# Kernel optimization log

Hardware: AMD Instinct MI355X
Metric: run time of the kernel (lower is better)

## Reference

```python
import jax, jax.numpy as jnp
import numpy as np

ALPHA = 0.15
KSIZE = 5
EPS = 1e-6


def _minmax_norm(x):
    # x: [B,1,H,W]; per-sample min-max normalize, 0.5 if nearly constant
    mn = x.min(axis=(1, 2, 3), keepdims=True)
    mx = x.max(axis=(1, 2, 3), keepdims=True)
    denom = mx - mn
    safe = jnp.where(denom > EPS, denom, 1.0)
    return jnp.where(denom > EPS, (x - mn) / safe, 0.5)


def _saliency_map(images, out_hw):
    # grayscale via luma weights
    w = jnp.array([0.299, 0.587, 0.114], dtype=images.dtype).reshape(1, 3, 1, 1)
    gray = (images * w).sum(axis=1, keepdims=True)  # [B,1,H,W]
    kernel = jnp.ones((1, 1, KSIZE, KSIZE), dtype=gray.dtype) / (KSIZE * KSIZE)
    dn = ('NCHW', 'OIHW', 'NCHW')
    local_mean = jax.lax.conv_general_dilated(gray, kernel, (1, 1), 'SAME', dimension_numbers=dn)
    local_mean_sq = jax.lax.conv_general_dilated(gray ** 2, kernel, (1, 1), 'SAME', dimension_numbers=dn)
    local_var = jnp.maximum(local_mean_sq - local_mean ** 2, 0.0)
    sal = _minmax_norm(local_var)
    if sal.shape[-2:] != out_hw:
        sal = jax.image.resize(sal, (sal.shape[0], 1, out_hw[0], out_hw[1]), method='bilinear')
    return jax.lax.stop_gradient(sal)  # computed under no_grad / detached in torch


def setup_inputs() -> dict:
    key = jax.random.key(0)
    k1, k2 = jax.random.split(key)
    features = jax.random.normal(k1, (64, 512, 28, 28), dtype=jnp.float32)
    images = jax.random.uniform(k2, (64, 3, 224, 224), dtype=jnp.float32)
    return {"features": features, "images": images}


def reference(features, images):
    sal = _saliency_map(images, features.shape[-2:])  # [B,1,Hf,Wf]
    attn = jnp.sqrt((features ** 2).mean(axis=1, keepdims=True))  # [B,1,Hf,Wf]
    attn = _minmax_norm(attn)
    loss = jnp.mean((attn - sal) ** 2)
    return ALPHA * loss
```

## Files before the change

kernel.cpp:

```cpp
#include <hip/hip_runtime.h>
#include <math.h>

#define BATCH 64
#define HIMG 224
#define WIMG 224
#define IMGPLANE (HIMG*WIMG)
#define CF 512
#define HF 28
#define WF 28
#define POS (HF*WF)
#define ALPHA_C 0.15f
#define EPS_C 1e-6f

#define STRIPS 14
#define SROWS 16
#define GROWS 20
#define GCOLS 228
#define GSTR 229
#define VSTR 261
#define SHN 4580

#define NATTN 512
#define NVARH (STRIPS*BATCH)

#define OFF_HRES 0
#define HRES_CNT (BATCH*HIMG*WF)
#define OFF_BMM (OFF_HRES + HRES_CNT)
#define OFF_AP  (OFF_BMM + BATCH*STRIPS*2)
#define OFF_ACC (OFF_AP + 8*BATCH*POS)
#define OFF_CNT (OFF_ACC + 1)

__global__ __launch_bounds__(256, 2) void fat_k(const float* __restrict__ img,
                                                const float* __restrict__ f,
                                                float* __restrict__ ws) {
    __shared__ float sh[SHN];
    __shared__ float wred[8];
    int bid = blockIdx.x;
    int tid = threadIdx.x;
    int g11 = bid / 11, r11 = bid - 11 * g11;

    if (r11 < 4) {
        int ab = g11 * 4 + r11;
        if (ab == 0 && tid == 0) {
            ws[OFF_ACC] = 0.0f;
            ((unsigned*)ws)[OFF_CNT] = 0u;
        }
        if (tid >= 196) return;
        int b = ab >> 3, z = ab & 7;
        const float* fp = f + (size_t)(b * CF + z * 64) * POS + 4 * tid;
        float ax = 0.0f, ay = 0.0f, az = 0.0f, aw = 0.0f;
        #pragma unroll
        for (int cc = 0; cc < 64; cc += 16) {
            float4 u[16];
            #pragma unroll
            for (int j = 0; j < 16; j++)
                u[j] = *(const float4*)(fp + (size_t)(cc + j) * POS);
            #pragma unroll
            for (int j = 0; j < 16; j++) {
                ax += u[j].x * u[j].x; ay += u[j].y * u[j].y;
                az += u[j].z * u[j].z; aw += u[j].w * u[j].w;
            }
        }
        float4 o = make_float4(ax, ay, az, aw);
        *(float4*)(ws + OFF_AP + (size_t)(z * BATCH + b) * POS + 4 * tid) = o;
        return;
    }

    int vb = g11 * 7 + (r11 - 4);
    int b = vb / STRIPS, sy = vb - b * STRIPS;
    int y0 = sy * SROWS;
    const float* imb = img + (size_t)b * 3 * IMGPLANE;

    for (int i = tid; i < GROWS * 56; i += 256) {
        int gr = i / 56, q = i - gr * 56;
        int gy = y0 - 2 + gr;
        float gx0 = 0.0f, gx1 = 0.0f, gx2 = 0.0f, gx3 = 0.0f;
        if ((unsigned)gy < HIMG) {
            const float* row = imb + gy * WIMG + 4 * q;
            float4 a = *(const float4*)(row);
            float4 bb = *(const float4*)(row + IMGPLANE);
            float4 c = *(const float4*)(row + 2 * IMGPLANE);
            gx0 = 0.299f * a.x + 0.587f * bb.x + 0.114f * c.x;
            gx1 = 0.299f * a.y + 0.587f * bb.y + 0.114f * c.y;
            gx2 = 0.299f * a.z + 0.587f * bb.z + 0.114f * c.z;
            gx3 = 0.299f * a.w + 0.587f * bb.w + 0.114f * c.w;
        }
        int base = gr * GSTR + 2 + 4 * q;
        sh[base] = gx0; sh[base + 1] = gx1; sh[base + 2] = gx2; sh[base + 3] = gx3;
    }
    if (tid < GROWS * 4) {
        int gr = tid >> 2, p = tid & 3;
        int gc = (p < 2) ? p : (224 + p);
        sh[gr * GSTR + gc] = 0.0f;
    }
    __syncthreads();

    int r = tid >> 4, s = tid & 15;
    int x0 = 14 * s;
    const float* gr0 = sh + r * GSTR;
    float c1[5], c2[5], vreg[14];
    #pragma unroll
    for (int m = 0; m < 5; m++) {
        float a = 0.0f, a2 = 0.0f;
        #pragma unroll
        for (int k = 0; k < 5; k++) {
            float u = gr0[k * GSTR + x0 + m];
            a += u; a2 += u * u;
        }
        c1[m] = a; c2[m] = a2;
    }
    float vmn = INFINITY, vmx = 0.0f;
    #pragma unroll
    for (int xi = 0; xi < 14; xi++) {
        int p = xi % 5;
        float s1 = c1[p], s2 = c2[p];
        #pragma unroll
        for (int m = 1; m < 5; m++) {
            s1 += c1[(p + m) % 5];
            s2 += c2[(p + m) % 5];
        }
        float m1 = s1 * 0.04f, m2 = s2 * 0.04f;
        float vv = fmaxf(m2 - m1 * m1, 0.0f);
        vreg[xi] = vv;
        vmn = fminf(vmn, vv); vmx = fmaxf(vmx, vv);
        if (xi < 13) {
            float a = 0.0f, a2 = 0.0f;
            #pragma unroll
            for (int k = 0; k < 5; k++) {
                float u = gr0[k * GSTR + x0 + xi + 5];
                a += u; a2 += u * u;
            }
            c1[p] = a; c2[p] = a2;
        }
    }
    #pragma unroll
    for (int o = 32; o > 0; o >>= 1) {
        vmn = fminf(vmn, __shfl_xor(vmn, o));
        vmx = fmaxf(vmx, __shfl_xor(vmx, o));
    }
    __syncthreads();
    int w = tid >> 6;
    if ((tid & 63) == 0) { wred[w] = vmn; wred[4 + w] = vmx; }
    if (tid < SROWS * 8) {
        int rr = tid >> 3, p = tid & 7;
        int jh = p + ((p < 4) ? 0 : 224);
        sh[rr * VSTR + jh + (jh >> 3)] = 0.0f;
    }
    #pragma unroll
    for (int xi = 0; xi < 14; xi++) {
        int jh = x0 + xi + 4;
        sh[r * VSTR + jh + (jh >> 3)] = vreg[xi];
    }
    __syncthreads();
    if (tid == 0) {
        float mn = fminf(fminf(wred[0], wred[1]), fminf(wred[2], wred[3]));
        float mx = fmaxf(fmaxf(wred[4], wred[5]), fmaxf(wred[6], wred[7]));
        int blk = b * STRIPS + sy;
        ws[OFF_BMM + 2 * blk]     = mn;
        ws[OFF_BMM + 2 * blk + 1] = mx;
    }

    float* hb = ws + OFF_HRES + ((size_t)b * HIMG + y0) * WF;
    for (int idx = tid; idx < SROWS * WF; idx += 256) {
        int rr = idx / WF, i = idx - rr * WF;
        float acc = 0.0f, wsum = 0.0f;
        int j0 = 8 * i - 4;
        #pragma unroll
        for (int t = 0; t < 16; t++) {
            int j = j0 + t;
            float w_ = 8.0f - fabsf((float)t - 7.5f);
            int jh = j + 4;
            acc += w_ * sh[rr * VSTR + jh + (jh >> 3)];
            if ((unsigned)j < WIMG) wsum += w_;
        }
        hb[idx] = acc / wsum;
    }
}

__global__ __launch_bounds__(256) void fused_k(float* __restrict__ ws,
                                               float* __restrict__ out) {
    __shared__ float hres[HIMG][WF + 1];
    __shared__ float wred[4];
    __shared__ float s_mn, s_mx;
    int b = blockIdx.x;
    int tid = threadIdx.x;

    if (tid < 64) {
        float mn = INFINITY, mx = 0.0f;
        if (tid < STRIPS) {
            mn = ws[OFF_BMM + 2 * (b * STRIPS + tid)];
            mx = ws[OFF_BMM + 2 * (b * STRIPS + tid) + 1];
        }
        #pragma unroll
        for (int o = 8; o > 0; o >>= 1) {
            mn = fminf(mn, __shfl_down(mn, o));
            mx = fmaxf(mx, __shfl_down(mx, o));
        }
        if (tid == 0) { s_mn = mn; s_mx = mx; }
    }

    const float* hg = ws + OFF_HRES + (size_t)b * HIMG * WF;
    for (int i = tid; i < HIMG * WF; i += 256) {
        int y = i / WF, x = i - y * WF;
        hres[y][x] = hg[i];
    }
    __syncthreads();

    float vmn = s_mn, vmx = s_mx;
    float vden = vmx - vmn;
    bool vok = vden > EPS_C;

    const float* ap = ws + OFF_AP + (size_t)b * POS;
    float salv[4], attnv[4];
    float amn = INFINITY, amx = -INFINITY;
    #pragma unroll
    for (int k = 0; k < 4; k++) {
        int idx = tid + 256 * k;
        salv[k] = 0.0f; attnv[k] = 0.0f;
        if (idx < POS) {
            int yo = idx / WF, x = idx - yo * WF;
            float acc = 0.0f, wsum = 0.0f;
            int j0 = 8 * yo - 4;
            #pragma unroll
            for (int t = 0; t < 16; t++) {
                int j = j0 + t;
                float w = 8.0f - fabsf((float)t - 7.5f);
                if ((unsigned)j < HIMG) { acc += w * hres[j][x]; wsum += w; }
            }
            float sraw = acc / wsum;
            salv[k] = vok ? (sraw - vmn) / vden : 0.5f;
            float ssum = 0.0f;
            #pragma unroll
            for (int z = 0; z < 8; z++)
                ssum += ap[(size_t)z * BATCH * POS + idx];
            float a = sqrtf(ssum * (1.0f / CF));
            attnv[k] = a;
            amn = fminf(amn, a); amx = fmaxf(amx, a);
        }
    }

    #pragma unroll
    for (int o = 32; o > 0; o >>= 1) {
        amn = fminf(amn, __shfl_xor(amn, o));
        amx = fmaxf(amx, __shfl_xor(amx, o));
    }
    int w = tid >> 6;
    if ((tid & 63) == 0) wred[w] = amn;
    __syncthreads();
    if (tid == 0) s_mn = fminf(fminf(wred[0], wred[1]), fminf(wred[2], wred[3]));
    __syncthreads();
    if ((tid & 63) == 0) wred[w] = amx;
    __syncthreads();
    if (tid == 0) s_mx = fmaxf(fmaxf(wred[0], wred[1]), fmaxf(wred[2], wred[3]));
    __syncthreads();
    amn = s_mn; amx = s_mx;
    float aden = amx - amn;
    bool aok = aden > EPS_C;

    float lsum = 0.0f;
    #pragma unroll
    for (int k = 0; k < 4; k++) {
        int idx = tid + 256 * k;
        if (idx < POS) {
            float an = aok ? (attnv[k] - amn) / aden : 0.5f;
            float d = an - salv[k];
            lsum += d * d;
        }
    }
    #pragma unroll
    for (int o = 32; o > 0; o >>= 1) lsum += __shfl_xor(lsum, o);
    if ((tid & 63) == 0) wred[w] = lsum;
    __syncthreads();

    if (tid == 0) {
        float part = wred[0] + wred[1] + wred[2] + wred[3];
        atomicAdd(ws + OFF_ACC, part);
        __threadfence();
        unsigned old = atomicAdd((unsigned*)ws + OFF_CNT, 1u);
        if (old == BATCH - 1) {
            float tot = atomicAdd(ws + OFF_ACC, 0.0f);
            out[0] = tot * (ALPHA_C / (float)(BATCH * POS));
        }
    }
}

extern "C" void kernel_launch(void* const* d_in, const int* in_sizes, int n_in,
                              void* d_out, int out_size, void* d_ws, size_t ws_size,
                              hipStream_t stream) {
    const float* features = (const float*)d_in[0];
    const float* images   = (const float*)d_in[1];
    float* ws  = (float*)d_ws;
    float* out = (float*)d_out;

    hipLaunchKernelGGL(fat_k,   dim3(NATTN + NVARH), dim3(256), 0, stream,
                       images, features, ws);
    hipLaunchKernelGGL(fused_k, dim3(BATCH),         dim3(256), 0, stream, ws, out);
}
```

Before: 191.0 us.

## Fuse finalize into main kernel using per-sample last-block counters

Removes the second kernel launch. Each sample now has an atomic completion counter, and the last of its 22 blocks (8 attention plus 14 saliency strips) does the bilinear resize, normalization and loss reduction. That lets per-sample finalization overlap with other samples' work. Image loads are batched into registers behind a sched_barrier to raise memory-level parallelism. The global float atomic is replaced by a deterministic last-block sum over per-sample partials. A hipMemsetAsync now zeroes the counters, and shared memory grows to hold the hres tile.

```diff
diff --git a/kernel.cpp b/kernel.cpp
--- a/kernel.cpp
+++ b/kernel.cpp
@@ -15,10 +15,10 @@
 #define STRIPS 14
 #define SROWS 16
 #define GROWS 20
-#define GCOLS 228
 #define GSTR 229
 #define VSTR 261
-#define SHN 4580
+#define HSTR 29
+#define SHN (HIMG*HSTR)
 
 #define NATTN 512
 #define NVARH (STRIPS*BATCH)
@@ -27,163 +27,184 @@
 #define HRES_CNT (BATCH*HIMG*WF)
 #define OFF_BMM (OFF_HRES + HRES_CNT)
 #define OFF_AP  (OFF_BMM + BATCH*STRIPS*2)
-#define OFF_ACC (OFF_AP + 8*BATCH*POS)
-#define OFF_CNT (OFF_ACC + 1)
+#define OFF_SCNT (OFF_AP + 8*BATCH*POS)
+#define OFF_GCNT (OFF_SCNT + BATCH)
 
 __global__ __launch_bounds__(256, 2) void fat_k(const float* __restrict__ img,
                                                 const float* __restrict__ f,
-                                                float* __restrict__ ws) {
+                                                float* __restrict__ ws,
+                                                float* __restrict__ out) {
     __shared__ float sh[SHN];
     __shared__ float wred[8];
+    __shared__ float s_mn, s_mx;
+    __shared__ int s_fin;
     int bid = blockIdx.x;
     int tid = threadIdx.x;
     int g11 = bid / 11, r11 = bid - 11 * g11;
+    int bsmp;
 
     if (r11 < 4) {
         int ab = g11 * 4 + r11;
-        if (ab == 0 && tid == 0) {
-            ws[OFF_ACC] = 0.0f;
-            ((unsigned*)ws)[OFF_CNT] = 0u;
-        }
-        if (tid >= 196) return;
-        int b = ab >> 3, z = ab & 7;
-        const float* fp = f + (size_t)(b * CF + z * 64) * POS + 4 * tid;
-        float ax = 0.0f, ay = 0.0f, az = 0.0f, aw = 0.0f;
-        #pragma unroll
-        for (int cc = 0; cc < 64; cc += 16) {
-            float4 u[16];
-            #pragma unroll
-            for (int j = 0; j < 16; j++)
-                u[j] = *(const float4*)(fp + (size_t)(cc + j) * POS);
-            #pragma unroll
-            for (int j = 0; j < 16; j++) {
-                ax += u[j].x * u[j].x; ay += u[j].y * u[j].y;
-                az += u[j].z * u[j].z; aw += u[j].w * u[j].w;
-            }
-        }
-        float4 o = make_float4(ax, ay, az, aw);
-        *(float4*)(ws + OFF_AP + (size_t)(z * BATCH + b) * POS + 4 * tid) = o;
-        return;
-    }
-
-    int vb = g11 * 7 + (r11 - 4);
-    int b = vb / STRIPS, sy = vb - b * STRIPS;
-    int y0 = sy * SROWS;
-    const float* imb = img + (size_t)b * 3 * IMGPLANE;
-
-    for (int i = tid; i < GROWS * 56; i += 256) {
-        int gr = i / 56, q = i - gr * 56;
-        int gy = y0 - 2 + gr;
-        float gx0 = 0.0f, gx1 = 0.0f, gx2 = 0.0f, gx3 = 0.0f;
-        if ((unsigned)gy < HIMG) {
-            const float* row = imb + gy * WIMG + 4 * q;
-            float4 a = *(const float4*)(row);
-            float4 bb = *(const float4*)(row + IMGPLANE);
-            float4 c = *(const float4*)(row + 2 * IMGPLANE);
-            gx0 = 0.299f * a.x + 0.587f * bb.x + 0.114f * c.x;
-            gx1 = 0.299f * a.y + 0.587f * bb.y + 0.114f * c.y;
-            gx2 = 0.299f * a.z + 0.587f * bb.z + 0.114f * c.z;
-            gx3 = 0.299f * a.w + 0.587f * bb.w + 0.114f * c.w;
-        }
-        int base = gr * GSTR + 2 + 4 * q;
-        sh[base] = gx0; sh[base + 1] = gx1; sh[base + 2] = gx2; sh[base + 3] = gx3;
-    }
-    if (tid < GROWS * 4) {
-        int gr = tid >> 2, p = tid & 3;
-        int gc = (p < 2) ? p : (224 + p);
-        sh[gr * GSTR + gc] = 0.0f;
-    }
-    __syncthreads();
-
-    int r = tid >> 4, s = tid & 15;
-    int x0 = 14 * s;
-    const float* gr0 = sh + r * GSTR;
-    float c1[5], c2[5], vreg[14];
-    #pragma unroll
-    for (int m = 0; m < 5; m++) {
-        float a = 0.0f, a2 = 0.0f;
-        #pragma unroll
-        for (int k = 0; k < 5; k++) {
-            float u = gr0[k * GSTR + x0 + m];
-            a += u; a2 += u * u;
-        }
-        c1[m] = a; c2[m] = a2;
-    }
-    float vmn = INFINITY, vmx = 0.0f;
-    #pragma unroll
-    for (int xi = 0; xi < 14; xi++) {
-        int p = xi % 5;
-        float s1 = c1[p], s2 = c2[p];
-        #pragma unroll
-        for (int m = 1; m < 5; m++) {
-            s1 += c1[(p + m) % 5];
-            s2 += c2[(p + m) % 5];
-        }
-        float m1 = s1 * 0.04f, m2 = s2 * 0.04f;
-        float vv = fmaxf(m2 - m1 * m1, 0.0f);
-        vreg[xi] = vv;
-        vmn = fminf(vmn, vv); vmx = fmaxf(vmx, vv);
-        if (xi < 13) {
+        bsmp = ab >> 3;
+        if (tid < 196) {
+            int z = ab & 7;
+            const float* fp = f + (size_t)(bsmp * CF + z * 64) * POS + 4 * tid;
+            float ax = 0.0f, ay = 0.0f, az = 0.0f, aw = 0.0f;
+            #pragma unroll
+            for (int cc = 0; cc < 64; cc += 16) {
+                float4 u[16];
+                #pragma unroll
+                for (int j = 0; j < 16; j++)
+                    u[j] = *(const float4*)(fp + (size_t)(cc + j) * POS);
+                __builtin_amdgcn_sched_barrier(0);
+                #pragma unroll
+                for (int j = 0; j < 16; j++) {
+                    ax += u[j].x * u[j].x; ay += u[j].y * u[j].y;
+                    az += u[j].z * u[j].z; aw += u[j].w * u[j].w;
+                }
+            }
+            float4 o = make_float4(ax, ay, az, aw);
+            *(float4*)(ws + OFF_AP + (size_t)(z * BATCH + bsmp) * POS + 4 * tid) = o;
+        }
+    } else {
+        int vb = g11 * 7 + (r11 - 4);
+        int b = vb / STRIPS, sy = vb - b * STRIPS;
+        bsmp = b;
+        int y0 = sy * SROWS;
+        const float* imb = img + (size_t)b * 3 * IMGPLANE;
+
+        float4 ua[5], ub[5], uc[5];
+        #pragma unroll
+        for (int it = 0; it < 5; ++it) {
+            int i = tid + 256 * it;
+            if (i < GROWS * 56) {
+                int gr = i / 56, q = i - gr * 56;
+                int gy = y0 - 2 + gr;
+                if ((unsigned)gy < HIMG) {
+                    const float* row = imb + gy * WIMG + 4 * q;
+                    ua[it] = *(const float4*)(row);
+                    ub[it] = *(const float4*)(row + IMGPLANE);
+                    uc[it] = *(const float4*)(row + 2 * IMGPLANE);
+                } else {
+                    ua[it] = make_float4(0.0f, 0.0f, 0.0f, 0.0f);
+                    ub[it] = ua[it]; uc[it] = ua[it];
+                }
+            }
+        }
+        __builtin_amdgcn_sched_barrier(0);
+        #pragma unroll
+        for (int it = 0; it < 5; ++it) {
+            int i = tid + 256 * it;
+            if (i < GROWS * 56) {
+                int gr = i / 56, q = i - gr * 56;
+                float4 a = ua[it], bb = ub[it], c = uc[it];
+                int base = gr * GSTR + 2 + 4 * q;
+                sh[base]     = 0.299f * a.x + 0.587f * bb.x + 0.114f * c.x;
+                sh[base + 1] = 0.299f * a.y + 0.587f * bb.y + 0.114f * c.y;
+                sh[base + 2] = 0.299f * a.z + 0.587f * bb.z + 0.114f * c.z;
+                sh[base + 3] = 0.299f * a.w + 0.587f * bb.w + 0.114f * c.w;
+            }
+        }
+        if (tid < GROWS * 4) {
+            int gr = tid >> 2, p = tid & 3;
+            int gc = (p < 2) ? p : (224 + p);
+            sh[gr * GSTR + gc] = 0.0f;
+        }
+        __syncthreads();
+
+        int r = tid >> 4, s = tid & 15;
+        int x0 = 14 * s;
+        const float* gr0 = sh + r * GSTR;
+        float c1[5], c2[5], vreg[14];
+        #pragma unroll
+        for (int m = 0; m < 5; m++) {
             float a = 0.0f, a2 = 0.0f;
             #pragma unroll
             for (int k = 0; k < 5; k++) {
-                float u = gr0[k * GSTR + x0 + xi + 5];
+                float u = gr0[k * GSTR + x0 + m];
                 a += u; a2 += u * u;
             }
-            c1[p] = a; c2[p] = a2;
-        }
-    }
-    #pragma unroll
-    for (int o = 32; o > 0; o >>= 1) {
-        vmn = fminf(vmn, __shfl_xor(vmn, o));
-        vmx = fmaxf(vmx, __shfl_xor(vmx, o));
-    }
-    __syncthreads();
-    int w = tid >> 6;
-    if ((tid & 63) == 0) { wred[w] = vmn; wred[4 + w] = vmx; }
-    if (tid < SROWS * 8) {
-        int rr = tid >> 3, p = tid & 7;
-        int jh = p + ((p < 4) ? 0 : 224);
-        sh[rr * VSTR + jh + (jh >> 3)] = 0.0f;
-    }
-    #pragma unroll
-    for (int xi = 0; xi < 14; xi++) {
-        int jh = x0 + xi + 4;
-        sh[r * VSTR + jh + (jh >> 3)] = vreg[xi];
-    }
+            c1[m] = a; c2[m] = a2;
+        }
+        float vmn = INFINITY, vmx = 0.0f;
+        #pragma unroll
+        for (int xi = 0; xi < 14; xi++) {
+            int p = xi % 5;
+            float s1 = c1[p], s2 = c2[p];
+            #pragma unroll
+            for (int m = 1; m < 5; m++) {
+                s1 += c1[(p + m) % 5];
+                s2 += c2[(p + m) % 5];
+            }
+            float m1 = s1 * 0.04f, m2 = s2 * 0.04f;
+            float vv = fmaxf(m2 - m1 * m1, 0.0f);
+            vreg[xi] = vv;
+            vmn = fminf(vmn, vv); vmx = fmaxf(vmx, vv);
+            if (xi < 13) {
+                float a = 0.0f, a2 = 0.0f;
+                #pragma unroll
+                for (int k = 0; k < 5; k++) {
+                    float u = gr0[k * GSTR + x0 + xi + 5];
+                    a += u; a2 += u * u;
+                }
+                c1[p] = a; c2[p] = a2;
+            }
+        }
+        #pragma unroll
+        for (int o = 32; o > 0; o >>= 1) {
+            vmn = fminf(vmn, __shfl_xor(vmn, o));
+            vmx = fmaxf(vmx, __shfl_xor(vmx, o));
+        }
+        __syncthreads();
+        int w = tid >> 6;
+        if ((tid & 63) == 0) { wred[w] = vmn; wred[4 + w] = vmx; }
+        if (tid < SROWS * 8) {
+            int rr = tid >> 3, p = tid & 7;
+            int jh = p + ((p < 4) ? 0 : 224);
+            sh[rr * VSTR + jh + (jh >> 3)] = 0.0f;
+        }
+        #pragma unroll
+        for (int xi = 0; xi < 14; xi++) {
+            int jh = x0 + xi + 4;
+            sh[r * VSTR + jh + (jh >> 3)] = vreg[xi];
+        }
+        __syncthreads();
+        if (tid == 0) {
+            float mn = fminf(fminf(wred[0], wred[1]), fminf(wred[2], wred[3]));
+            float mx = fmaxf(fmaxf(wred[4], wred[5]), fmaxf(wred[6], wred[7]));
+            int blk = b * STRIPS + sy;
+            ws[OFF_BMM + 2 * blk]     = mn;
+            ws[OFF_BMM + 2 * blk + 1] = mx;
+        }
+
+        float* hb = ws + OFF_HRES + ((size_t)b * HIMG + y0) * WF;
+        for (int idx = tid; idx < SROWS * WF; idx += 256) {
+            int rr = idx / WF, i = idx - rr * WF;
+            float acc = 0.0f, wsum = 0.0f;
+            int j0 = 8 * i - 4;
+            #pragma unroll
+            for (int t = 0; t < 16; t++) {
+                int j = j0 + t;
+                float w_ = 8.0f - fabsf((float)t - 7.5f);
+                int jh = j + 4;
+                acc += w_ * sh[rr * VSTR + jh + (jh >> 3)];
+                if ((unsigned)j < WIMG) wsum += w_;
+            }
+            hb[idx] = acc / wsum;
+        }
+    }
+
     __syncthreads();
     if (tid == 0) {
-        float mn = fminf(fminf(wred[0], wred[1]), fminf(wred[2], wred[3]));
-        float mx = fmaxf(fmaxf(wred[4], wred[5]), fmaxf(wred[6], wred[7]));
-        int blk = b * STRIPS + sy;
-        ws[OFF_BMM + 2 * blk]     = mn;
-        ws[OFF_BMM + 2 * blk + 1] = mx;
-    }
-
-    float* hb = ws + OFF_HRES + ((size_t)b * HIMG + y0) * WF;
-    for (int idx = tid; idx < SROWS * WF; idx += 256) {
-        int rr = idx / WF, i = idx - rr * WF;
-        float acc = 0.0f, wsum = 0.0f;
-        int j0 = 8 * i - 4;
-        #pragma unroll
-        for (int t = 0; t < 16; t++) {
-            int j = j0 + t;
-            float w_ = 8.0f - fabsf((float)t - 7.5f);
-            int jh = j + 4;
-            acc += w_ * sh[rr * VSTR + jh + (jh >> 3)];
-            if ((unsigned)j < WIMG) wsum += w_;
-        }
-        hb[idx] = acc / wsum;
-    }
-}
-
-__global__ __launch_bounds__(256) void fused_k(float* __restrict__ ws,
-                                               float* __restrict__ out) {
-    __shared__ float hres[HIMG][WF + 1];
-    __shared__ float wred[4];
-    __shared__ float s_mn, s_mx;
-    int b = blockIdx.x;
-    int tid = threadIdx.x;
+        __threadfence();
+        unsigned old = atomicAdd((unsigned*)ws + OFF_SCNT + bsmp, 1u);
+        s_fin = (old == 21u) ? 1 : 0;
+    }
+    __syncthreads();
+    if (!s_fin) return;
+    __threadfence();
+
+    int b = bsmp;
 
     if (tid < 64) {
         float mn = INFINITY, mx = 0.0f;
@@ -200,9 +221,11 @@
     }
 
     const float* hg = ws + OFF_HRES + (size_t)b * HIMG * WF;
-    for (int i = tid; i < HIMG * WF; i += 256) {
-        int y = i / WF, x = i - y * WF;
-        hres[y][x] = hg[i];
+    for (int i4 = tid; i4 < HIMG * 7; i4 += 256) {
+        float4 v = ((const float4*)hg)[i4];
+        int y = i4 / 7, x4 = (i4 - y * 7) * 4;
+        float* d = sh + y * HSTR + x4;
+        d[0] = v.x; d[1] = v.y; d[2] = v.z; d[3] = v.w;
     }
     __syncthreads();
 
@@ -224,8 +247,8 @@
             #pragma unroll
             for (int t = 0; t < 16; t++) {
                 int j = j0 + t;
-                float w = 8.0f - fabsf((float)t - 7.5f);
-                if ((unsigned)j < HIMG) { acc += w * hres[j][x]; wsum += w; }
+                float wt = 8.0f - fabsf((float)t - 7.5f);
+                if ((unsigned)j < HIMG) { acc += wt * sh[j * HSTR + x]; wsum += wt; }
             }
             float sraw = acc / wsum;
             salv[k] = vok ? (sraw - vmn) / vden : 0.5f;
@@ -244,12 +267,12 @@
         amn = fminf(amn, __shfl_xor(amn, o));
         amx = fmaxf(amx, __shfl_xor(amx, o));
     }
-    int w = tid >> 6;
-    if ((tid & 63) == 0) wred[w] = amn;
+    int wv = tid >> 6;
+    if ((tid & 63) == 0) wred[wv] = amn;
     __syncthreads();
     if (tid == 0) s_mn = fminf(fminf(wred[0], wred[1]), fminf(wred[2], wred[3]));
     __syncthreads();
-    if ((tid & 63) == 0) wred[w] = amx;
+    if ((tid & 63) == 0) wred[wv] = amx;
     __syncthreads();
     if (tid == 0) s_mx = fmaxf(fmaxf(wred[0], wred[1]), fmaxf(wred[2], wred[3]));
     __syncthreads();
@@ -269,18 +292,23 @@
     }
     #pragma unroll
     for (int o = 32; o > 0; o >>= 1) lsum += __shfl_xor(lsum, o);
-    if ((tid & 63) == 0) wred[w] = lsum;
+    if ((tid & 63) == 0) wred[wv] = lsum;
     __syncthreads();
 
     if (tid == 0) {
         float part = wred[0] + wred[1] + wred[2] + wred[3];
-        atomicAdd(ws + OFF_ACC, part);
+        ws[OFF_BMM + 28 * b] = part;
         __threadfence();
-        unsigned old = atomicAdd((unsigned*)ws + OFF_CNT, 1u);
-        if (old == BATCH - 1) {
-            float tot = atomicAdd(ws + OFF_ACC, 0.0f);
-            out[0] = tot * (ALPHA_C / (float)(BATCH * POS));
-        }
+        unsigned old = atomicAdd((unsigned*)ws + OFF_GCNT, 1u);
+        s_fin = (old == BATCH - 1) ? 1 : 0;
+    }
+    __syncthreads();
+    if (s_fin && tid < 64) {
+        __threadfence();
+        float v = ws[OFF_BMM + 28 * tid];
+        #pragma unroll
+        for (int o = 32; o > 0; o >>= 1) v += __shfl_xor(v, o);
+        if (tid == 0) out[0] = v * (ALPHA_C / (float)(BATCH * POS));
     }
 }
 
@@ -292,7 +320,8 @@
     float* ws  = (float*)d_ws;
     float* out = (float*)d_out;
 
-    hipLaunchKernelGGL(fat_k,   dim3(NATTN + NVARH), dim3(256), 0, stream,
-                       images, features, ws);
-    hipLaunchKernelGGL(fused_k, dim3(BATCH),         dim3(256), 0, stream, ws, out);
+    hipMemsetAsync((char*)d_ws + (size_t)OFF_SCNT * sizeof(float), 0,
+                   (BATCH + 1) * sizeof(unsigned), stream);
+    hipLaunchKernelGGL(fat_k, dim3(NATTN + NVARH), dim3(256), 0, stream,
+                       images, features, ws, out);
 }
```

Result: slower. 284.3 us (+48.8%).

## Split fused attention/variance kernel into separate attention and variance launches

Applied to the files above, without the earlier changes.

Splits the previously interleaved heterogeneous kernel into a dedicated attention-energy kernel with fully packed 256-thread blocks (no idle threads) and a separate variance kernel, then the existing reduction kernel. The attention kernel adds a scheduling barrier to group the loads ahead of the FMAs and sets a waves-per-EU hint. This removes the 60 idle threads per attention block and lets each kernel be compiled for its own register needs, at the cost of an extra launch and losing the concurrent overlap of the memory-bound feature reads with the image stencil work.

```diff
diff --git a/kernel.cpp b/kernel.cpp
--- a/kernel.cpp
+++ b/kernel.cpp
@@ -15,13 +15,12 @@
 #define STRIPS 14
 #define SROWS 16
 #define GROWS 20
-#define GCOLS 228
 #define GSTR 229
 #define VSTR 261
 #define SHN 4580
 
-#define NATTN 512
 #define NVARH (STRIPS*BATCH)
+#define NATTNB 392
 
 #define OFF_HRES 0
 #define HRES_CNT (BATCH*HIMG*WF)
@@ -30,43 +29,42 @@
 #define OFF_ACC (OFF_AP + 8*BATCH*POS)
 #define OFF_CNT (OFF_ACC + 1)
 
-__global__ __launch_bounds__(256, 2) void fat_k(const float* __restrict__ img,
-                                                const float* __restrict__ f,
-                                                float* __restrict__ ws) {
+__global__ __attribute__((amdgpu_flat_work_group_size(256, 256),
+                          amdgpu_waves_per_eu(2, 4)))
+void attn_k(const float* __restrict__ f, float* __restrict__ ws) {
+    int t = blockIdx.x * 256 + threadIdx.x;
+    if (t == 0) {
+        ws[OFF_ACC] = 0.0f;
+        ((unsigned*)ws)[OFF_CNT] = 0u;
+    }
+    int b = t / 1568;
+    int rem = t - b * 1568;
+    int z = rem / 196, q = rem - z * 196;
+    const float* fp = f + (size_t)(b * CF + z * 64) * POS + 4 * q;
+    float ax = 0.0f, ay = 0.0f, az = 0.0f, aw = 0.0f;
+    #pragma unroll
+    for (int cc = 0; cc < 64; cc += 16) {
+        float4 u[16];
+        #pragma unroll
+        for (int j = 0; j < 16; j++)
+            u[j] = *(const float4*)(fp + (size_t)(cc + j) * POS);
+        __builtin_amdgcn_sched_barrier(0);
+        #pragma unroll
+        for (int j = 0; j < 16; j++) {
+            ax += u[j].x * u[j].x; ay += u[j].y * u[j].y;
+            az += u[j].z * u[j].z; aw += u[j].w * u[j].w;
+        }
+    }
+    float4 o = make_float4(ax, ay, az, aw);
+    *(float4*)(ws + OFF_AP + (size_t)(z * BATCH + b) * POS + 4 * q) = o;
+}
+
+__global__ __launch_bounds__(256, 2) void varh_k(const float* __restrict__ img,
+                                                 float* __restrict__ ws) {
     __shared__ float sh[SHN];
     __shared__ float wred[8];
-    int bid = blockIdx.x;
+    int vb = blockIdx.x;
     int tid = threadIdx.x;
-    int g11 = bid / 11, r11 = bid - 11 * g11;
-
-    if (r11 < 4) {
-        int ab = g11 * 4 + r11;
-        if (ab == 0 && tid == 0) {
-            ws[OFF_ACC] = 0.0f;
-            ((unsigned*)ws)[OFF_CNT] = 0u;
-        }
-        if (tid >= 196) return;
-        int b = ab >> 3, z = ab & 7;
-        const float* fp = f + (size_t)(b * CF + z * 64) * POS + 4 * tid;
-        float ax = 0.0f, ay = 0.0f, az = 0.0f, aw = 0.0f;
-        #pragma unroll
-        for (int cc = 0; cc < 64; cc += 16) {
-            float4 u[16];
-            #pragma unroll
-            for (int j = 0; j < 16; j++)
-                u[j] = *(const float4*)(fp + (size_t)(cc + j) * POS);
-            #pragma unroll
-            for (int j = 0; j < 16; j++) {
-                ax += u[j].x * u[j].x; ay += u[j].y * u[j].y;
-                az += u[j].z * u[j].z; aw += u[j].w * u[j].w;
-            }
-        }
-        float4 o = make_float4(ax, ay, az, aw);
-        *(float4*)(ws + OFF_AP + (size_t)(z * BATCH + b) * POS + 4 * tid) = o;
-        return;
-    }
-
-    int vb = g11 * 7 + (r11 - 4);
     int b = vb / STRIPS, sy = vb - b * STRIPS;
     int y0 = sy * SROWS;
     const float* imb = img + (size_t)b * 3 * IMGPLANE;
@@ -292,7 +290,7 @@
     float* ws  = (float*)d_ws;
     float* out = (float*)d_out;
 
-    hipLaunchKernelGGL(fat_k,   dim3(NATTN + NVARH), dim3(256), 0, stream,
-                       images, features, ws);
-    hipLaunchKernelGGL(fused_k, dim3(BATCH),         dim3(256), 0, stream, ws, out);
-}
+    hipLaunchKernelGGL(attn_k, dim3(NATTNB), dim3(256), 0, stream, features, ws);
+    hipLaunchKernelGGL(varh_k, dim3(NVARH),  dim3(256), 0, stream, images, ws);
+    hipLaunchKernelGGL(fused_k, dim3(BATCH), dim3(256), 0, stream, ws, out);
+}
```

Result: no change. 193.9 us (+1.5%).

## Fuse per-sample finalize into main kernel via last-block-done counters

Applied to the files above, without the earlier changes.

Removes the second kernel. Each sample now has an atomic counter that all 22 of its blocks (8 attention, 14 saliency strips) bump when they finish, and the last block runs the per-sample normalize and loss itself, reading the horizontally resized rows from global memory instead of staging them in LDS. Feature and image loads become nontemporal, the channel loop is simplified, and the counters are cleared with a memset before the launch. The intent is to drop a kernel launch and the tail it creates, at the cost of a serial finalize inside whichever block arrives last and uncached global reads.

```diff
diff --git a/kernel.cpp b/kernel.cpp
--- a/kernel.cpp
+++ b/kernel.cpp
@@ -15,7 +15,6 @@
 #define STRIPS 14
 #define SROWS 16
 #define GROWS 20
-#define GCOLS 228
 #define GSTR 229
 #define VSTR 261
 #define SHN 4580
@@ -25,165 +24,171 @@
 
 #define OFF_HRES 0
 #define HRES_CNT (BATCH*HIMG*WF)
-#define OFF_BMM (OFF_HRES + HRES_CNT)
-#define OFF_AP  (OFF_BMM + BATCH*STRIPS*2)
-#define OFF_ACC (OFF_AP + 8*BATCH*POS)
-#define OFF_CNT (OFF_ACC + 1)
+#define OFF_BMM  (OFF_HRES + HRES_CNT)
+#define OFF_AP   (OFF_BMM + BATCH*STRIPS*2)
+#define OFF_ACC  (OFF_AP + 8*BATCH*POS)
+#define OFF_CNT  (OFF_ACC + 1)
+#define OFF_SCNT (OFF_CNT + 1)
+
+typedef float f4v __attribute__((ext_vector_type(4)));
+
+__device__ __forceinline__ f4v nt4(const float* p) {
+    return __builtin_nontemporal_load((const f4v*)p);
+}
 
 __global__ __launch_bounds__(256, 2) void fat_k(const float* __restrict__ img,
                                                 const float* __restrict__ f,
-                                                float* __restrict__ ws) {
+                                                float* __restrict__ ws,
+                                                float* __restrict__ out) {
     __shared__ float sh[SHN];
     __shared__ float wred[8];
+    __shared__ float s_mn, s_mx;
+    __shared__ int s_fin;
     int bid = blockIdx.x;
     int tid = threadIdx.x;
     int g11 = bid / 11, r11 = bid - 11 * g11;
+    int bsmp;
 
     if (r11 < 4) {
         int ab = g11 * 4 + r11;
-        if (ab == 0 && tid == 0) {
-            ws[OFF_ACC] = 0.0f;
-            ((unsigned*)ws)[OFF_CNT] = 0u;
-        }
-        if (tid >= 196) return;
-        int b = ab >> 3, z = ab & 7;
-        const float* fp = f + (size_t)(b * CF + z * 64) * POS + 4 * tid;
-        float ax = 0.0f, ay = 0.0f, az = 0.0f, aw = 0.0f;
-        #pragma unroll
-        for (int cc = 0; cc < 64; cc += 16) {
-            float4 u[16];
-            #pragma unroll
-            for (int j = 0; j < 16; j++)
-                u[j] = *(const float4*)(fp + (size_t)(cc + j) * POS);
-            #pragma unroll
-            for (int j = 0; j < 16; j++) {
-                ax += u[j].x * u[j].x; ay += u[j].y * u[j].y;
-                az += u[j].z * u[j].z; aw += u[j].w * u[j].w;
-            }
-        }
-        float4 o = make_float4(ax, ay, az, aw);
-        *(float4*)(ws + OFF_AP + (size_t)(z * BATCH + b) * POS + 4 * tid) = o;
-        return;
-    }
-
-    int vb = g11 * 7 + (r11 - 4);
-    int b = vb / STRIPS, sy = vb - b * STRIPS;
-    int y0 = sy * SROWS;
-    const float* imb = img + (size_t)b * 3 * IMGPLANE;
-
-    for (int i = tid; i < GROWS * 56; i += 256) {
-        int gr = i / 56, q = i - gr * 56;
-        int gy = y0 - 2 + gr;
-        float gx0 = 0.0f, gx1 = 0.0f, gx2 = 0.0f, gx3 = 0.0f;
-        if ((unsigned)gy < HIMG) {
-            const float* row = imb + gy * WIMG + 4 * q;
-            float4 a = *(const float4*)(row);
-            float4 bb = *(const float4*)(row + IMGPLANE);
-            float4 c = *(const float4*)(row + 2 * IMGPLANE);
-            gx0 = 0.299f * a.x + 0.587f * bb.x + 0.114f * c.x;
-            gx1 = 0.299f * a.y + 0.587f * bb.y + 0.114f * c.y;
-            gx2 = 0.299f * a.z + 0.587f * bb.z + 0.114f * c.z;
-            gx3 = 0.299f * a.w + 0.587f * bb.w + 0.114f * c.w;
-        }
-        int base = gr * GSTR + 2 + 4 * q;
-        sh[base] = gx0; sh[base + 1] = gx1; sh[base + 2] = gx2; sh[base + 3] = gx3;
-    }
-    if (tid < GROWS * 4) {
-        int gr = tid >> 2, p = tid & 3;
-        int gc = (p < 2) ? p : (224 + p);
-        sh[gr * GSTR + gc] = 0.0f;
-    }
-    __syncthreads();
-
-    int r = tid >> 4, s = tid & 15;
-    int x0 = 14 * s;
-    const float* gr0 = sh + r * GSTR;
-    float c1[5], c2[5], vreg[14];
-    #pragma unroll
-    for (int m = 0; m < 5; m++) {
-        float a = 0.0f, a2 = 0.0f;
-        #pragma unroll
-        for (int k = 0; k < 5; k++) {
-            float u = gr0[k * GSTR + x0 + m];
-            a += u; a2 += u * u;
-        }
-        c1[m] = a; c2[m] = a2;
-    }
-    float vmn = INFINITY, vmx = 0.0f;
-    #pragma unroll
-    for (int xi = 0; xi < 14; xi++) {
-        int p = xi % 5;
-        float s1 = c1[p], s2 = c2[p];
-        #pragma unroll
-        for (int m = 1; m < 5; m++) {
-            s1 += c1[(p + m) % 5];
-            s2 += c2[(p + m) % 5];
-        }
-        float m1 = s1 * 0.04f, m2 = s2 * 0.04f;
-        float vv = fmaxf(m2 - m1 * m1, 0.0f);
-        vreg[xi] = vv;
-        vmn = fminf(vmn, vv); vmx = fmaxf(vmx, vv);
-        if (xi < 13) {
+        bsmp = ab >> 3;
+        if (tid < 196) {
+            int z = ab & 7;
+            const float* fp = f + (size_t)(bsmp * CF + z * 64) * POS + 4 * tid;
+            float ax = 0.0f, ay = 0.0f, az = 0.0f, aw = 0.0f;
+            #pragma unroll
+            for (int c = 0; c < 64; c++) {
+                f4v u = nt4(fp + (size_t)c * POS);
+                ax += u.x * u.x; ay += u.y * u.y;
+                az += u.z * u.z; aw += u.w * u.w;
+            }
+            float4 o = make_float4(ax, ay, az, aw);
+            *(float4*)(ws + OFF_AP + (size_t)((ab & 7) * BATCH + bsmp) * POS + 4 * tid) = o;
+        }
+    } else {
+        int vb = g11 * 7 + (r11 - 4);
+        int b = vb / STRIPS, sy = vb - b * STRIPS;
+        bsmp = b;
+        int y0 = sy * SROWS;
+        const float* imb = img + (size_t)b * 3 * IMGPLANE;
+
+        for (int i = tid; i < GROWS * 56; i += 256) {
+            int gr = i / 56, q = i - gr * 56;
+            int gy = y0 - 2 + gr;
+            float gx0 = 0.0f, gx1 = 0.0f, gx2 = 0.0f, gx3 = 0.0f;
+            if ((unsigned)gy < HIMG) {
+                const float* row = imb + gy * WIMG + 4 * q;
+                f4v a = nt4(row);
+                f4v bb = nt4(row + IMGPLANE);
+                f4v c = nt4(row + 2 * IMGPLANE);
+                gx0 = 0.299f * a.x + 0.587f * bb.x + 0.114f * c.x;
+                gx1 = 0.299f * a.y + 0.587f * bb.y + 0.114f * c.y;
+                gx2 = 0.299f * a.z + 0.587f * bb.z + 0.114f * c.z;
+                gx3 = 0.299f * a.w + 0.587f * bb.w + 0.114f * c.w;
+            }
+            int base = gr * GSTR + 2 + 4 * q;
+            sh[base] = gx0; sh[base + 1] = gx1; sh[base + 2] = gx2; sh[base + 3] = gx3;
+        }
+        if (tid < GROWS * 4) {
+            int gr = tid >> 2, p = tid & 3;
+            int gc = (p < 2) ? p : (224 + p);
+            sh[gr * GSTR + gc] = 0.0f;
+        }
+        __syncthreads();
+
+        int r = tid >> 4, s = tid & 15;
+        int x0 = 14 * s;
+        const float* gr0 = sh + r * GSTR;
+        float c1[5], c2[5], vreg[14];
+        #pragma unroll
+        for (int m = 0; m < 5; m++) {
             float a = 0.0f, a2 = 0.0f;
             #pragma unroll
             for (int k = 0; k < 5; k++) {
-                float u = gr0[k * GSTR + x0 + xi + 5];
+                float u = gr0[k * GSTR + x0 + m];
                 a += u; a2 += u * u;
             }
-            c1[p] = a; c2[p] = a2;
-        }
-    }
-    #pragma unroll
-    for (int o = 32; o > 0; o >>= 1) {
-        vmn = fminf(vmn, __shfl_xor(vmn, o));
-        vmx = fmaxf(vmx, __shfl_xor(vmx, o));
-    }
-    __syncthreads();
-    int w = tid >> 6;
-    if ((tid & 63) == 0) { wred[w] = vmn; wred[4 + w] = vmx; }
-    if (tid < SROWS * 8) {
-        int rr = tid >> 3, p = tid & 7;
-        int jh = p + ((p < 4) ? 0 : 224);
-        sh[rr * VSTR + jh + (jh >> 3)] = 0.0f;
-    }
-    #pragma unroll
-    for (int xi = 0; xi < 14; xi++) {
-        int jh = x0 + xi + 4;
-        sh[r * VSTR + jh + (jh >> 3)] = vreg[xi];
-    }
+            c1[m] = a; c2[m] = a2;
+        }
+        float vmn = INFINITY, vmx = 0.0f;
+        #pragma unroll
+        for (int xi = 0; xi < 14; xi++) {
+            int p = xi % 5;
+            float s1 = c1[p], s2 = c2[p];
+            #pragma unroll
+            for (int m = 1; m < 5; m++) {
+                s1 += c1[(p + m) % 5];
+                s2 += c2[(p + m) % 5];
+            }
+            float m1 = s1 * 0.04f, m2 = s2 * 0.04f;
+            float vv = fmaxf(m2 - m1 * m1, 0.0f);
+            vreg[xi] = vv;
+            vmn = fminf(vmn, vv); vmx = fmaxf(vmx, vv);
+            if (xi < 13) {
+                float a = 0.0f, a2 = 0.0f;
+                #pragma unroll
+                for (int k = 0; k < 5; k++) {
+                    float u = gr0[k * GSTR + x0 + xi + 5];
+                    a += u; a2 += u * u;
+                }
+                c1[p] = a; c2[p] = a2;
+            }
+        }
+        #pragma unroll
+        for (int o = 32; o > 0; o >>= 1) {
+            vmn = fminf(vmn, __shfl_xor(vmn, o));
+            vmx = fmaxf(vmx, __shfl_xor(vmx, o));
+        }
+        __syncthreads();
+        int w = tid >> 6;
+        if ((tid & 63) == 0) { wred[w] = vmn; wred[4 + w] = vmx; }
+        if (tid < SROWS * 8) {
+            int rr = tid >> 3, p = tid & 7;
+            int jh = p + ((p < 4) ? 0 : 224);
+            sh[rr * VSTR + jh + (jh >> 3)] = 0.0f;
+        }
+        #pragma unroll
+        for (int xi = 0; xi < 14; xi++) {
+            int jh = x0 + xi + 4;
+            sh[r * VSTR + jh + (jh >> 3)] = vreg[xi];
+        }
+        __syncthreads();
+        if (tid == 0) {
+            float mn = fminf(fminf(wred[0], wred[1]), fminf(wred[2], wred[3]));
+            float mx = fmaxf(fmaxf(wred[4], wred[5]), fmaxf(wred[6], wred[7]));
+            int blk = b * STRIPS + sy;
+            ws[OFF_BMM + 2 * blk]     = mn;
+            ws[OFF_BMM + 2 * blk + 1] = mx;
+        }
+
+        float* hb = ws + OFF_HRES + ((size_t)b * HIMG + y0) * WF;
+        for (int idx = tid; idx < SROWS * WF; idx += 256) {
+            int rr = idx / WF, i = idx - rr * WF;
+            float acc = 0.0f, wsum = 0.0f;
+            int j0 = 8 * i - 4;
+            #pragma unroll
+            for (int t = 0; t < 16; t++) {
+                int j = j0 + t;
+                float w_ = 8.0f - fabsf((float)t - 7.5f);
+                int jh = j + 4;
+                acc += w_ * sh[rr * VSTR + jh + (jh >> 3)];
+                if ((unsigned)j < WIMG) wsum += w_;
+            }
+            hb[idx] = acc / wsum;
+        }
+    }
+
     __syncthreads();
     if (tid == 0) {
-        float mn = fminf(fminf(wred[0], wred[1]), fminf(wred[2], wred[3]));
-        float mx = fmaxf(fmaxf(wred[4], wred[5]), fmaxf(wred[6], wred[7]));
-        int blk = b * STRIPS + sy;
-        ws[OFF_BMM + 2 * blk]     = mn;
-        ws[OFF_BMM + 2 * blk + 1] = mx;
-    }
-
-    float* hb = ws + OFF_HRES + ((size_t)b * HIMG + y0) * WF;
-    for (int idx = tid; idx < SROWS * WF; idx += 256) {
-        int rr = idx / WF, i = idx - rr * WF;
-        float acc = 0.0f, wsum = 0.0f;
-        int j0 = 8 * i - 4;
-        #pragma unroll
-        for (int t = 0; t < 16; t++) {
-            int j = j0 + t;
-            float w_ = 8.0f - fabsf((float)t - 7.5f);
-            int jh = j + 4;
-            acc += w_ * sh[rr * VSTR + jh + (jh >> 3)];
-            if ((unsigned)j < WIMG) wsum += w_;
-        }
-        hb[idx] = acc / wsum;
-    }
-}
-
-__global__ __launch_bounds__(256) void fused_k(float* __restrict__ ws,
-                                               float* __restrict__ out) {
-    __shared__ float hres[HIMG][WF + 1];
-    __shared__ float wred[4];
-    __shared__ float s_mn, s_mx;
-    int b = blockIdx.x;
-    int tid = threadIdx.x;
+        __threadfence();
+        unsigned old = atomicAdd((unsigned*)ws + OFF_SCNT + bsmp, 1u);
+        s_fin = (old == 21u) ? 1 : 0;
+    }
+    __syncthreads();
+    if (!s_fin) return;
+    __threadfence();
+
+    int b = bsmp;
 
     if (tid < 64) {
         float mn = INFINITY, mx = 0.0f;
@@ -198,18 +203,12 @@
         }
         if (tid == 0) { s_mn = mn; s_mx = mx; }
     }
-
-    const float* hg = ws + OFF_HRES + (size_t)b * HIMG * WF;
-    for (int i = tid; i < HIMG * WF; i += 256) {
-        int y = i / WF, x = i - y * WF;
-        hres[y][x] = hg[i];
-    }
-    __syncthreads();
-
+    __syncthreads();
     float vmn = s_mn, vmx = s_mx;
     float vden = vmx - vmn;
     bool vok = vden > EPS_C;
 
+    const float* hg = ws + OFF_HRES + (size_t)b * HIMG * WF;
     const float* ap = ws + OFF_AP + (size_t)b * POS;
     float salv[4], attnv[4];
     float amn = INFINITY, amx = -INFINITY;
@@ -225,7 +224,7 @@
             for (int t = 0; t < 16; t++) {
                 int j = j0 + t;
                 float w = 8.0f - fabsf((float)t - 7.5f);
-                if ((unsigned)j < HIMG) { acc += w * hres[j][x]; wsum += w; }
+                if ((unsigned)j < HIMG) { acc += w * hg[j * WF + x]; wsum += w; }
             }
             float sraw = acc / wsum;
             salv[k] = vok ? (sraw - vmn) / vden : 0.5f;
@@ -244,14 +243,13 @@
         amn = fminf(amn, __shfl_xor(amn, o));
         amx = fmaxf(amx, __shfl_xor(amx, o));
     }
-    int w = tid >> 6;
-    if ((tid & 63) == 0) wred[w] = amn;
-    __syncthreads();
-    if (tid == 0) s_mn = fminf(fminf(wred[0], wred[1]), fminf(wred[2], wred[3]));
-    __syncthreads();
-    if ((tid & 63) == 0) wred[w] = amx;
-    __syncthreads();
-    if (tid == 0) s_mx = fmaxf(fmaxf(wred[0], wred[1]), fmaxf(wred[2], wred[3]));
+    int wv = tid >> 6;
+    if ((tid & 63) == 0) { wred[wv] = amn; wred[4 + wv] = amx; }
+    __syncthreads();
+    if (tid == 0) {
+        s_mn = fminf(fminf(wred[0], wred[1]), fminf(wred[2], wred[3]));
+        s_mx = fmaxf(fmaxf(wred[4], wred[5]), fmaxf(wred[6], wred[7]));
+    }
     __syncthreads();
     amn = s_mn; amx = s_mx;
     float aden = amx - amn;
@@ -269,7 +267,7 @@
     }
     #pragma unroll
     for (int o = 32; o > 0; o >>= 1) lsum += __shfl_xor(lsum, o);
-    if ((tid & 63) == 0) wred[w] = lsum;
+    if ((tid & 63) == 0) wred[wv] = lsum;
     __syncthreads();
 
     if (tid == 0) {
@@ -292,7 +290,8 @@
     float* ws  = (float*)d_ws;
     float* out = (float*)d_out;
 
-    hipLaunchKernelGGL(fat_k,   dim3(NATTN + NVARH), dim3(256), 0, stream,
-                       images, features, ws);
-    hipLaunchKernelGGL(fused_k, dim3(BATCH),         dim3(256), 0, stream, ws, out);
+    hipMemsetAsync((char*)d_ws + (size_t)OFF_ACC * sizeof(float), 0,
+                   (2 + BATCH) * sizeof(unsigned), stream);
+    hipLaunchKernelGGL(fat_k, dim3(NATTN + NVARH), dim3(256), 0, stream,
+                       images, features, ws, out);
 }
```

Measured after the change: 277.6 us. 1.45x slower.
